# Kernel optimization log

Measured on AMD Instinct MI355X. Metric: run time of the kernel, lower is better.

The kernel has to match this reference:

```python
import jax, jax.numpy as jnp
import numpy as np

B, S, C, H = 2, 4096, 1024, 8
D = C // H
KCONV = 7  # depthwise causal conv kernel size


def setup_inputs() -> dict:
    key = jax.random.key(0)
    k1, k2, k3, k4 = jax.random.split(key, 4)
    x = jax.random.normal(k1, (B, S, C), jnp.float32)
    Wqkv = jax.random.normal(k2, (C, 3 * C), jnp.float32) * (1.0 / np.sqrt(C))
    Wo = jax.random.normal(k3, (C, C), jnp.float32) * (1.0 / np.sqrt(C))
    conv_w = jax.random.normal(k4, (C, KCONV), jnp.float32) * (1.0 / np.sqrt(KCONV))
    return {"x": x, "Wqkv": Wqkv, "Wo": Wo, "conv_w": conv_w}


def _ripple(x, Wqkv, Wo, conv_w):
    b, s, c = x.shape
    d = c // H
    qkv = x @ Wqkv
    q, k, v = jnp.split(qkv, 3, axis=-1)

    def heads(t):
        return t.reshape(b, s, H, d).transpose(0, 2, 1, 3)  # [B,H,S,D]

    qh, kh, vh = heads(q), heads(k), heads(v)

    # --- branch 1: telescoping attention (offsets 0, 1, 2, 4, ..., 2^k) ---
    n_pow = int(np.floor(np.log2(s))) + 1
    offsets = jnp.concatenate([jnp.zeros((1,), jnp.int32),
                               (2 ** jnp.arange(n_pow)).astype(jnp.int32)])  # [K]
    pos = jnp.arange(s, dtype=jnp.int32)[:, None] - offsets[None, :]  # [S,K]
    valid = pos >= 0
    posc = jnp.clip(pos, 0)
    kg = kh[:, :, posc]  # [B,H,S,K,D] gathered keys
    vg = vh[:, :, posc]  # [B,H,S,K,D] gathered values
    sc = jnp.einsum('bhsd,bhskd->bhsk', qh, kg) / np.sqrt(d)
    sc = jnp.where(valid[None, None], sc, -jnp.inf)  # offset 0 always valid
    w = jax.nn.softmax(sc, axis=-1)
    tele = jnp.einsum('bhsk,bhskd->bhsd', w, vg)

    # --- branch 2: depthwise causal conv over value stream ---
    vpad = jnp.pad(v, ((0, 0), (KCONV - 1, 0), (0, 0)))  # left pad -> causal
    conv = jax.lax.conv_general_dilated(
        vpad.transpose(0, 2, 1),        # NCH
        conv_w[:, None, :],             # OIH, groups=C -> I=1
        window_strides=(1,), padding='VALID',
        feature_group_count=c,
        dimension_numbers=('NCH', 'OIH', 'NCH')).transpose(0, 2, 1)  # [B,S,C]
    conv_h = conv.reshape(b, s, H, d).transpose(0, 2, 1, 3)

    # --- branch 3: low-rank (linear) attention, elu+1 feature map ---
    fq = jax.nn.elu(qh) + 1.0
    fk = jax.nn.elu(kh) + 1.0
    kv = jnp.einsum('bhsd,bhse->bhde', fk, vh)        # [B,H,D,D]
    z = jnp.einsum('bhsd,bhd->bhs', fq, fk.sum(2))    # normalizer
    low = jnp.einsum('bhsd,bhde->bhse', fq, kv) / (z[..., None] + 1e-6)

    h = (tele + conv_h + low).transpose(0, 2, 1, 3).reshape(b, s, c)
    return h @ Wo


def reference(x, Wqkv, Wo, conv_w):
    # RippleAttentionBlock: h, _ = ripple_attn(x); return x + h
    return x + _ripple(x, Wqkv, Wo, conv_w)
```

## Files before the change

kernel.cpp:

```cpp
#include <hip/hip_runtime.h>
#include <hip/hip_bf16.h>

#define BATCH 2
#define SEQ   4096
#define CHN   1024
#define NH    8
#define HD    128
#define NQROWS (BATCH*SEQ)
#define QKVN  (3*CHN)
#define NOFF  14
#define KCONV 7
#define NCH   16
#define CHS   (SEQ/NCH)
#define SLICE ((size_t)SEQ*HD)

typedef short bf16x8v __attribute__((ext_vector_type(8)));
typedef short bf16x4v __attribute__((ext_vector_type(4)));
typedef float f32x4v  __attribute__((ext_vector_type(4)));

__device__ __forceinline__ float b2f(short s) {
    return __uint_as_float(((unsigned)(unsigned short)s) << 16);
}
__device__ __forceinline__ unsigned short f2bu(float f) {
    __hip_bfloat16 h = __float2bfloat16(f);
    return *reinterpret_cast<unsigned short*>(&h);
}
__device__ __forceinline__ void gload16(const void* g, void* l) {
    __builtin_amdgcn_global_load_lds(
        (const __attribute__((address_space(1))) unsigned int*)g,
        (__attribute__((address_space(3))) unsigned int*)l, 16, 0, 0);
}

__global__ void k_cvt(const float* __restrict__ in, short* __restrict__ out, int n4) {
    int i = blockIdx.x * blockDim.x + threadIdx.x;
    int stride = gridDim.x * blockDim.x;
    for (; i < n4; i += stride) {
        float4 v = reinterpret_cast<const float4*>(in)[i];
        ushort4 o;
        o.x = f2bu(v.x); o.y = f2bu(v.y); o.z = f2bu(v.z); o.w = f2bu(v.w);
        reinterpret_cast<ushort4*>(out)[i] = o;
    }
}

__global__ void k_transpose_cvt(const float* __restrict__ in, short* __restrict__ out,
                                int R, int Cc) {
    __shared__ float tile[32][33];
    int bc = blockIdx.x * 32, br = blockIdx.y * 32;
    int tx = threadIdx.x & 31, ty = threadIdx.x >> 5;
    for (int i = 0; i < 32; i += 8)
        tile[ty + i][tx] = in[(size_t)(br + ty + i) * Cc + bc + tx];
    __syncthreads();
    for (int i = 0; i < 32; i += 8)
        out[(size_t)(bc + ty + i) * R + br + tx] = (short)f2bu(tile[tx][ty + i]);
}

template<int EPI>
__global__ __launch_bounds__(256)
void k_gemm_bt(const short* __restrict__ A, const short* __restrict__ Bt,
               short* __restrict__ Cb, float* __restrict__ Cf,
               const float* __restrict__ resid, int M, int N, int K) {
    __shared__ short As[128 * 32];
    __shared__ short Bs[128 * 32];
    int tid = threadIdx.x;
    int w = tid >> 6, lane = tid & 63;
    int nbn = N >> 7;
    int bm = blockIdx.x / nbn, bn = blockIdx.x % nbn;
    size_t m0 = (size_t)bm << 7, n0 = (size_t)bn << 7;
    int wr = (w >> 1) << 6, wc = (w & 1) << 6;
    int lr = lane & 15, lk = lane >> 4;
    f32x4v acc[4][4] = {};

    int f0 = w * 64 + lane, f1 = f0 + 256;
    int r0 = f0 >> 2, q0 = f0 & 3;
    int r1 = f1 >> 2, q1 = f1 & 3;
    const short* Ap0 = A + (m0 + r0) * K + q0 * 8;
    const short* Ap1 = A + (m0 + r1) * K + q1 * 8;
    const short* Bp0 = Bt + (n0 + r0) * K + q0 * 8;
    const short* Bp1 = Bt + (n0 + r1) * K + q1 * 8;
    short* Asl0 = As + (w * 64) * 8;
    short* Asl1 = As + (256 + w * 64) * 8;
    short* Bsl0 = Bs + (w * 64) * 8;
    short* Bsl1 = Bs + (256 + w * 64) * 8;

    for (int k0 = 0; k0 < K; k0 += 32) {
        gload16(Ap0 + k0, Asl0);
        gload16(Ap1 + k0, Asl1);
        gload16(Bp0 + k0, Bsl0);
        gload16(Bp1 + k0, Bsl1);
        __syncthreads();
        bf16x8v af[4], bfv[4];
        #pragma unroll
        for (int m = 0; m < 4; ++m)
            af[m] = *reinterpret_cast<const bf16x8v*>(As + (wr + m * 16 + lr) * 32 + lk * 8);
        #pragma unroll
        for (int n = 0; n < 4; ++n)
            bfv[n] = *reinterpret_cast<const bf16x8v*>(Bs + (wc + n * 16 + lr) * 32 + lk * 8);
        #pragma unroll
        for (int m = 0; m < 4; ++m)
            #pragma unroll
            for (int n = 0; n < 4; ++n)
                acc[m][n] = __builtin_amdgcn_mfma_f32_16x16x32_bf16(af[m], bfv[n], acc[m][n], 0, 0, 0);
        __syncthreads();
    }
    #pragma unroll
    for (int m = 0; m < 4; ++m) {
        size_t grow = m0 + wr + m * 16 + lk * 4;
        #pragma unroll
        for (int n = 0; n < 4; ++n) {
            size_t gcol = n0 + wc + n * 16 + lr;
            if (EPI == 0) {
                int bq = (int)(grow >> 12);
                int tq = (int)(gcol >> 10);
                int hh = ((int)gcol >> 7) & 7;
                int d  = (int)gcol & 127;
                size_t base = ((size_t)(tq * 2 + bq) * 8 + hh) * SLICE + d;
                #pragma unroll
                for (int i = 0; i < 4; ++i) {
                    size_t s = (grow + i) & 4095;
                    Cb[base + s * 128] = (short)f2bu(acc[m][n][i]);
                }
            } else {
                #pragma unroll
                for (int i = 0; i < 4; ++i) {
                    size_t idx = (grow + i) * N + gcol;
                    Cf[idx] = resid[idx] + acc[m][n][i];
                }
            }
        }
    }
}

__global__ __launch_bounds__(256)
void k_kvpart(const short* __restrict__ qkvs, float* __restrict__ kvpart,
              float* __restrict__ kspart) {
    __shared__ float fk_lds[32 * 128];
    __shared__ short v_lds[32 * 64];
    int t = threadIdx.x;
    int w = t >> 6, lane = t & 63;
    int bid = blockIdx.x;
    int eh = bid & 1;
    int ch = (bid >> 1) & (NCH - 1);
    int bh = bid / (NCH * 2);
    int b = bh >> 3, h = bh & 7;
    const short* kbase = qkvs + ((size_t)(2 + b) * 8 + h) * SLICE;
    const short* vbase = qkvs + ((size_t)(4 + b) * 8 + h) * SLICE + eh * 64;
    int s0 = ch * CHS;
    int d0 = (t >> 4) * 8;
    int e0l = (t & 15) * 4;
    float kv[8][4] = {};
    float ks[8] = {};
    for (int sub = 0; sub < CHS / 32; ++sub) {
        #pragma unroll
        for (int j = 0; j < 2; ++j) {
            int f = j * 256 + t;
            int row = f >> 4, c0 = (f & 15) * 8;
            bf16x8v k8 = *reinterpret_cast<const bf16x8v*>(
                kbase + (size_t)(s0 + sub * 32 + row) * HD + c0);
            float* dst = fk_lds + row * 128 + c0;
            #pragma unroll
            for (int e = 0; e < 8; ++e) {
                float x = b2f(k8[e]);
                dst[e] = x > 0.f ? x + 1.f : __expf(x);
            }
        }
        {
            int f = w * 64 + lane;
            gload16(vbase + (size_t)(s0 + sub * 32 + (f >> 3)) * HD + (f & 7) * 8,
                    v_lds + (size_t)(w * 64) * 8);
        }
        __syncthreads();
        for (int ss = 0; ss < 32; ++ss) {
            float fa[8];
            *(float4*)&fa[0] = *(const float4*)&fk_lds[ss * 128 + d0];
            *(float4*)&fa[4] = *(const float4*)&fk_lds[ss * 128 + d0 + 4];
            bf16x4v vv = *reinterpret_cast<const bf16x4v*>(&v_lds[ss * 64 + e0l]);
            float vb[4];
            #pragma unroll
            for (int e = 0; e < 4; ++e) vb[e] = b2f(vv[e]);
            #pragma unroll
            for (int i = 0; i < 8; ++i) {
                ks[i] += fa[i];
                #pragma unroll
                for (int e = 0; e < 4; ++e) kv[i][e] += fa[i] * vb[e];
            }
        }
        __syncthreads();
    }
    size_t obase = (size_t)bid * (128 * 64);
    #pragma unroll
    for (int i = 0; i < 8; ++i)
        *(float4*)&kvpart[obase + (d0 + i) * 64 + e0l] = *(float4*)&kv[i][0];
    if ((t & 15) == 0 && eh == 0)
        #pragma unroll
        for (int i = 0; i < 8; ++i)
            kspart[(size_t)(bh * NCH + ch) * 128 + d0 + i] = ks[i];
}

__global__ void k_kvreduce(const float* __restrict__ kvpart, const float* __restrict__ kspart,
                           short* __restrict__ kvt, float* __restrict__ ksum) {
    int idx = blockIdx.x * blockDim.x + threadIdx.x;
    const int total_kv = 16 * 128 * 128;
    if (idx < total_kv) {
        int bh = idx >> 14;
        int r = idx & 16383;
        int d = r >> 7, e = r & 127;
        int ehalf = e >> 6, el = e & 63;
        float s = 0.f;
        const float* p = kvpart + ((size_t)(bh * NCH) * 2 + ehalf) * 8192 + d * 64 + el;
        #pragma unroll
        for (int c = 0; c < NCH; ++c) s += p[(size_t)c * 2 * 8192];
        kvt[((size_t)bh << 14) + e * 128 + d] = (short)f2bu(s);
    } else {
        int k = idx - total_kv;
        if (k < 16 * 128) {
            int bh = k >> 7, d = k & 127;
            float s = 0.f;
            const float* p = kspart + (size_t)bh * NCH * 128 + d;
            #pragma unroll
            for (int c = 0; c < NCH; ++c) s += p[c * 128];
            ksum[k] = s;
        }
    }
}

__global__ __launch_bounds__(256)
void k_middle(const short* __restrict__ qkvs, const short* __restrict__ kvt,
              const float* __restrict__ ksum, const float* __restrict__ conv_w,
              short* __restrict__ hbuf) {
    __shared__ short fq_lds[32 * 128];
    __shared__ float low_lds[32 * 128];
    __shared__ float ksum_lds[128];
    __shared__ float cw_lds[128 * KCONV];
    int t = threadIdx.x;
    int w = t >> 6, lane = t & 63;
    int bid = blockIdx.x;
    int bh = bid >> 7, chunk = bid & 127;
    int b = bh >> 3, h = bh & 7;
    int s0 = chunk * 32;
    const short* qbase = qkvs + ((size_t)(0 + b) * 8 + h) * SLICE;
    const short* kbase = qkvs + ((size_t)(2 + b) * 8 + h) * SLICE;
    const short* vbase = qkvs + ((size_t)(4 + b) * 8 + h) * SLICE;

    if (t < 128) ksum_lds[t] = ksum[bh * 128 + t];
    for (int f = t; f < 128 * KCONV; f += 256) {
        int d = f / KCONV, j = f % KCONV;
        cw_lds[f] = conv_w[(h * HD + d) * KCONV + j];
    }
    #pragma unroll
    for (int j = 0; j < 2; ++j) {
        int f = j * 256 + t;
        int row = f >> 4, c0 = (f & 15) * 8;
        bf16x8v q8 = *reinterpret_cast<const bf16x8v*>(
            qbase + (size_t)(s0 + row) * HD + c0);
        bf16x8v fq8;
        #pragma unroll
        for (int e = 0; e < 8; ++e) {
            float x = b2f(q8[e]);
            float fx = x > 0.f ? x + 1.f : __expf(x);
            fq8[e] = (short)f2bu(fx);
        }
        *reinterpret_cast<bf16x8v*>(fq_lds + row * 128 + c0) = fq8;
    }
    __syncthreads();
    {
        int lr = lane & 15, lk = lane >> 4;
        const short* kvg = kvt + ((size_t)bh << 14);
        f32x4v lacc[2][2] = {};
        #pragma unroll
        for (int ksb = 0; ksb < 4; ++ksb) {
            bf16x8v af[2], bfv[2];
            #pragma unroll
            for (int m = 0; m < 2; ++m)
                af[m] = *reinterpret_cast<const bf16x8v*>(fq_lds + (m * 16 + lr) * 128 + ksb * 32 + lk * 8);
            #pragma unroll
            for (int n = 0; n < 2; ++n)
                bfv[n] = *reinterpret_cast<const bf16x8v*>(kvg + (w * 32 + n * 16 + lr) * 128 + ksb * 32 + lk * 8);
            #pragma unroll
            for (int m = 0; m < 2; ++m)
                #pragma unroll
                for (int n = 0; n < 2; ++n)
                    lacc[m][n] = __builtin_amdgcn_mfma_f32_16x16x32_bf16(af[m], bfv[n], lacc[m][n], 0, 0, 0);
        }
        #pragma unroll
        for (int m = 0; m < 2; ++m)
            #pragma unroll
            for (int n = 0; n < 2; ++n)
                #pragma unroll
                for (int i = 0; i < 4; ++i)
                    low_lds[(m * 16 + lk * 4 + i) * 128 + w * 32 + n * 16 + lr] = lacc[m][n][i];
    }
    int row = t >> 3, j8 = t & 7;
    int e0 = j8 * 16;
    int sl = s0 + row;
    float zp = 0.f;
    #pragma unroll
    for (int d = 0; d < 16; ++d)
        zp += b2f(fq_lds[row * 128 + e0 + d]) * ksum_lds[e0 + d];
    zp += __shfl_xor(zp, 1); zp += __shfl_xor(zp, 2); zp += __shfl_xor(zp, 4);
    float z = zp + 1e-6f;
    float qv[16];
    {
        const short* qp = qbase + (size_t)sl * HD + e0;
        bf16x8v q0 = *(const bf16x8v*)qp;
        bf16x8v q1 = *(const bf16x8v*)(qp + 8);
        #pragma unroll
        for (int d = 0; d < 8; ++d) { qv[d] = b2f(q0[d]); qv[8 + d] = b2f(q1[d]); }
    }
    float scb[NOFF];
    #pragma unroll
    for (int o = 0; o < NOFF; ++o) {
        int off = (o == 0) ? 0 : (1 << (o - 1));
        int p = sl - off;
        float acc = 0.f;
        if (p >= 0) {
            const short* kp = kbase + (size_t)p * HD + e0;
            bf16x8v k0v = *(const bf16x8v*)kp;
            bf16x8v k1v = *(const bf16x8v*)(kp + 8);
            #pragma unroll
            for (int d = 0; d < 8; ++d) acc += qv[d] * b2f(k0v[d]);
            #pragma unroll
            for (int d = 0; d < 8; ++d) acc += qv[8 + d] * b2f(k1v[d]);
        }
        scb[o] = acc;
    }
    #pragma unroll
    for (int o = 0; o < NOFF; ++o) {
        float v = scb[o];
        v += __shfl_xor(v, 1); v += __shfl_xor(v, 2); v += __shfl_xor(v, 4);
        scb[o] = v * 0.08838834764831845f;
    }
    float mmax = -1e30f;
    #pragma unroll
    for (int o = 0; o < NOFF; ++o) {
        int off = (o == 0) ? 0 : (1 << (o - 1));
        if (sl - off >= 0 && scb[o] > mmax) mmax = scb[o];
    }
    float wsum = 0.f;
    float tacc[16] = {};
    #pragma unroll
    for (int o = 0; o < NOFF; ++o) {
        int off = (o == 0) ? 0 : (1 << (o - 1));
        int p = sl - off;
        if (p < 0) continue;
        float wv = __expf(scb[o] - mmax);
        wsum += wv;
        const short* vp = vbase + (size_t)p * HD + e0;
        bf16x8v v0 = *(const bf16x8v*)vp;
        bf16x8v v1 = *(const bf16x8v*)(vp + 8);
        #pragma unroll
        for (int d = 0; d < 8; ++d) tacc[d]     += wv * b2f(v0[d]);
        #pragma unroll
        for (int d = 0; d < 8; ++d) tacc[8 + d] += wv * b2f(v1[d]);
    }
    float inv_wsum = 1.f / wsum;
    float cacc[16] = {};
    #pragma unroll
    for (int jj = 0; jj < KCONV; ++jj) {
        int p = sl - 6 + jj;
        if (p < 0) continue;
        const short* vp = vbase + (size_t)p * HD + e0;
        bf16x8v v0 = *(const bf16x8v*)vp;
        bf16x8v v1 = *(const bf16x8v*)(vp + 8);
        #pragma unroll
        for (int d = 0; d < 8; ++d) cacc[d]     += b2f(v0[d]) * cw_lds[(e0 + d) * KCONV + jj];
        #pragma unroll
        for (int d = 0; d < 8; ++d) cacc[8 + d] += b2f(v1[d]) * cw_lds[(e0 + 8 + d) * KCONV + jj];
    }
    __syncthreads();
    short outv[16];
    #pragma unroll
    for (int d = 0; d < 16; ++d) {
        float hval = tacc[d] * inv_wsum + cacc[d] + low_lds[row * 128 + e0 + d] / z;
        outv[d] = (short)f2bu(hval);
    }
    bf16x8v* op = (bf16x8v*)(hbuf + ((size_t)b * SEQ + sl) * CHN + h * HD + e0);
    op[0] = *(bf16x8v*)&outv[0];
    op[1] = *(bf16x8v*)&outv[8];
}

extern "C" void kernel_launch(void* const* d_in, const int* in_sizes, int n_in,
                              void* d_out, int out_size, void* d_ws, size_t ws_size,
                              hipStream_t stream) {
    const float* x      = (const float*)d_in[0];
    const float* Wqkv   = (const float*)d_in[1];
    const float* Wo     = (const float*)d_in[2];
    const float* conv_w = (const float*)d_in[3];
    float* out = (float*)d_out;

    char* ws = (char*)d_ws;
    size_t off = 0;
    auto alloc = [&](size_t bytes) {
        char* p = ws + off;
        off += (bytes + 255) & ~(size_t)255;
        return (void*)p;
    };
    short* xb     = (short*)alloc((size_t)NQROWS * CHN * 2);
    short* wqkvT  = (short*)alloc((size_t)QKVN * CHN * 2);
    short* woT    = (short*)alloc((size_t)CHN * CHN * 2);
    short* qkvs   = (short*)alloc((size_t)3 * BATCH * NH * SEQ * HD * 2);
    short* hbuf   = (short*)alloc((size_t)NQROWS * CHN * 2);
    float* kvpart = (float*)alloc((size_t)16 * NCH * 2 * 128 * 64 * 4);
    float* kspart = (float*)alloc((size_t)16 * NCH * 128 * 4);
    short* kvt    = (short*)alloc((size_t)16 * 128 * 128 * 2);
    float* ksum   = (float*)alloc((size_t)16 * 128 * 4);

    k_cvt<<<2048, 256, 0, stream>>>(x, xb, NQROWS * CHN / 4);
    k_transpose_cvt<<<dim3(QKVN / 32, CHN / 32), 256, 0, stream>>>(Wqkv, wqkvT, CHN, QKVN);
    k_transpose_cvt<<<dim3(CHN / 32, CHN / 32), 256, 0, stream>>>(Wo, woT, CHN, CHN);
    k_gemm_bt<0><<<(NQROWS / 128) * (QKVN / 128), 256, 0, stream>>>(
        xb, wqkvT, qkvs, nullptr, nullptr, NQROWS, QKVN, CHN);
    k_kvpart<<<16 * NCH * 2, 256, 0, stream>>>(qkvs, kvpart, kspart);
    k_kvreduce<<<(16 * 128 * 128 + 16 * 128) / 256, 256, 0, stream>>>(kvpart, kspart, kvt, ksum);
    k_middle<<<16 * 128, 256, 0, stream>>>(qkvs, kvt, ksum, conv_w, hbuf);
    k_gemm_bt<1><<<(NQROWS / 128) * (CHN / 128), 256, 0, stream>>>(
        hbuf, woT, nullptr, out, x, NQROWS, CHN, CHN);
}
```

Measured before the change: 298.9 us.

## Compute linear-attention KV partials with MFMA and split ksum into separate kernel

Replaces the scalar FMA outer-product KV accumulation with a bf16 MFMA kernel. It stages transposed, XOR-swizzled feature-mapped keys and values in LDS, uses 32 sequence chunks, and writes full 128x128 partials. The key-sum normalizer moves to its own small kernel. Both GEMMs are split into two launches over half the rows each via an m_off parameter. Feeding the feature-mapped keys to the MFMA as bf16 loses some precision, the KV partial buffer grows, and the split GEMMs add launch overhead.

```diff
diff --git a/kernel.cpp b/kernel.cpp
--- a/kernel.cpp
+++ b/kernel.cpp
@@ -10,12 +10,11 @@
 #define QKVN  (3*CHN)
 #define NOFF  14
 #define KCONV 7
-#define NCH   16
-#define CHS   (SEQ/NCH)
+#define NCH2  32
+#define CHS2  (SEQ/NCH2)
 #define SLICE ((size_t)SEQ*HD)
 
 typedef short bf16x8v __attribute__((ext_vector_type(8)));
-typedef short bf16x4v __attribute__((ext_vector_type(4)));
 typedef float f32x4v  __attribute__((ext_vector_type(4)));
 
 __device__ __forceinline__ float b2f(short s) {
@@ -58,14 +57,14 @@
 __global__ __launch_bounds__(256)
 void k_gemm_bt(const short* __restrict__ A, const short* __restrict__ Bt,
                short* __restrict__ Cb, float* __restrict__ Cf,
-               const float* __restrict__ resid, int M, int N, int K) {
+               const float* __restrict__ resid, int N, int K, int m_off) {
     __shared__ short As[128 * 32];
     __shared__ short Bs[128 * 32];
     int tid = threadIdx.x;
     int w = tid >> 6, lane = tid & 63;
     int nbn = N >> 7;
     int bm = blockIdx.x / nbn, bn = blockIdx.x % nbn;
-    size_t m0 = (size_t)bm << 7, n0 = (size_t)bn << 7;
+    size_t m0 = ((size_t)bm << 7) + m_off, n0 = (size_t)bn << 7;
     int wr = (w >> 1) << 6, wc = (w & 1) << 6;
     int lr = lane & 15, lk = lane >> 4;
     f32x4v acc[4][4] = {};
@@ -131,69 +130,84 @@
 }
 
 __global__ __launch_bounds__(256)
-void k_kvpart(const short* __restrict__ qkvs, float* __restrict__ kvpart,
-              float* __restrict__ kspart) {
-    __shared__ float fk_lds[32 * 128];
-    __shared__ short v_lds[32 * 64];
+void k_kvpart_mfma(const short* __restrict__ qkvs, float* __restrict__ kvpart) {
+    __shared__ short fkt[128 * 32];
+    __shared__ short vt[128 * 32];
     int t = threadIdx.x;
     int w = t >> 6, lane = t & 63;
+    int lr = lane & 15, lk = lane >> 4;
+    int bh = blockIdx.x >> 5, ch = blockIdx.x & 31;
+    int b = bh >> 3, h = bh & 7;
+    const short* kb = qkvs + ((size_t)(2 + b) * 8 + h) * SLICE;
+    const short* vb = qkvs + ((size_t)(4 + b) * 8 + h) * SLICE;
+    int s0 = ch * CHS2;
+    int dq = (w >> 1) * 64, eq = (w & 1) * 64;
+    int g16 = (t & 7) * 16;
+    int sl  = t >> 3;
+    f32x4v acc[4][4] = {};
+
+    for (int sub = 0; sub < CHS2 / 32; ++sub) {
+        int srow = s0 + sub * 32 + sl;
+        const short* kp = kb + (size_t)srow * HD + g16;
+        const short* vp = vb + (size_t)srow * HD + g16;
+        bf16x8v k0 = *(const bf16x8v*)kp, k1 = *(const bf16x8v*)(kp + 8);
+        bf16x8v v0 = *(const bf16x8v*)vp, v1 = *(const bf16x8v*)(vp + 8);
+        #pragma unroll
+        for (int jj = 0; jj < 16; ++jj) {
+            int d = g16 + jj;
+            float kx = b2f(jj < 8 ? k0[jj] : k1[jj - 8]);
+            float fkv = kx > 0.f ? kx + 1.f : __expf(kx);
+            int byte = (d * 64 + sl * 2) ^ ((jj & 7) << 4);
+            *(short*)((char*)fkt + byte) = (short)f2bu(fkv);
+            *(short*)((char*)vt  + byte) = (jj < 8 ? v0[jj] : v1[jj - 8]);
+        }
+        __syncthreads();
+        bf16x8v af[4], bfv[4];
+        #pragma unroll
+        for (int m = 0; m < 4; ++m) {
+            int byte = ((dq + m * 16 + lr) * 64 + lk * 16) ^ ((lr & 7) << 4);
+            af[m] = *(const bf16x8v*)((const char*)fkt + byte);
+        }
+        #pragma unroll
+        for (int n = 0; n < 4; ++n) {
+            int byte = ((eq + n * 16 + lr) * 64 + lk * 16) ^ ((lr & 7) << 4);
+            bfv[n] = *(const bf16x8v*)((const char*)vt + byte);
+        }
+        #pragma unroll
+        for (int m = 0; m < 4; ++m)
+            #pragma unroll
+            for (int n = 0; n < 4; ++n)
+                acc[m][n] = __builtin_amdgcn_mfma_f32_16x16x32_bf16(af[m], bfv[n], acc[m][n], 0, 0, 0);
+        __syncthreads();
+    }
+    size_t obase = (size_t)blockIdx.x * 16384;
+    #pragma unroll
+    for (int m = 0; m < 4; ++m) {
+        int dr = dq + m * 16 + lk * 4;
+        #pragma unroll
+        for (int n = 0; n < 4; ++n) {
+            int ec = eq + n * 16 + lr;
+            #pragma unroll
+            for (int i = 0; i < 4; ++i)
+                kvpart[obase + (size_t)(dr + i) * 128 + ec] = acc[m][n][i];
+        }
+    }
+}
+
+__global__ __launch_bounds__(128)
+void k_ksum(const short* __restrict__ qkvs, float* __restrict__ kspart) {
     int bid = blockIdx.x;
-    int eh = bid & 1;
-    int ch = (bid >> 1) & (NCH - 1);
-    int bh = bid / (NCH * 2);
+    int bh = bid >> 4, cs = bid & 15;
     int b = bh >> 3, h = bh & 7;
-    const short* kbase = qkvs + ((size_t)(2 + b) * 8 + h) * SLICE;
-    const short* vbase = qkvs + ((size_t)(4 + b) * 8 + h) * SLICE + eh * 64;
-    int s0 = ch * CHS;
-    int d0 = (t >> 4) * 8;
-    int e0l = (t & 15) * 4;
-    float kv[8][4] = {};
-    float ks[8] = {};
-    for (int sub = 0; sub < CHS / 32; ++sub) {
-        #pragma unroll
-        for (int j = 0; j < 2; ++j) {
-            int f = j * 256 + t;
-            int row = f >> 4, c0 = (f & 15) * 8;
-            bf16x8v k8 = *reinterpret_cast<const bf16x8v*>(
-                kbase + (size_t)(s0 + sub * 32 + row) * HD + c0);
-            float* dst = fk_lds + row * 128 + c0;
-            #pragma unroll
-            for (int e = 0; e < 8; ++e) {
-                float x = b2f(k8[e]);
-                dst[e] = x > 0.f ? x + 1.f : __expf(x);
-            }
-        }
-        {
-            int f = w * 64 + lane;
-            gload16(vbase + (size_t)(s0 + sub * 32 + (f >> 3)) * HD + (f & 7) * 8,
-                    v_lds + (size_t)(w * 64) * 8);
-        }
-        __syncthreads();
-        for (int ss = 0; ss < 32; ++ss) {
-            float fa[8];
-            *(float4*)&fa[0] = *(const float4*)&fk_lds[ss * 128 + d0];
-            *(float4*)&fa[4] = *(const float4*)&fk_lds[ss * 128 + d0 + 4];
-            bf16x4v vv = *reinterpret_cast<const bf16x4v*>(&v_lds[ss * 64 + e0l]);
-            float vb[4];
-            #pragma unroll
-            for (int e = 0; e < 4; ++e) vb[e] = b2f(vv[e]);
-            #pragma unroll
-            for (int i = 0; i < 8; ++i) {
-                ks[i] += fa[i];
-                #pragma unroll
-                for (int e = 0; e < 4; ++e) kv[i][e] += fa[i] * vb[e];
-            }
-        }
-        __syncthreads();
-    }
-    size_t obase = (size_t)bid * (128 * 64);
-    #pragma unroll
-    for (int i = 0; i < 8; ++i)
-        *(float4*)&kvpart[obase + (d0 + i) * 64 + e0l] = *(float4*)&kv[i][0];
-    if ((t & 15) == 0 && eh == 0)
-        #pragma unroll
-        for (int i = 0; i < 8; ++i)
-            kspart[(size_t)(bh * NCH + ch) * 128 + d0 + i] = ks[i];
+    int d = threadIdx.x;
+    const short* kb = qkvs + ((size_t)(2 + b) * 8 + h) * SLICE + (size_t)(cs * 256) * HD;
+    float s = 0.f;
+    #pragma unroll 4
+    for (int i = 0; i < 256; ++i) {
+        float x = b2f(kb[(size_t)i * HD + d]);
+        s += x > 0.f ? x + 1.f : __expf(x);
+    }
+    kspart[bid * 128 + d] = s;
 }
 
 __global__ void k_kvreduce(const float* __restrict__ kvpart, const float* __restrict__ kspart,
@@ -204,20 +218,19 @@
         int bh = idx >> 14;
         int r = idx & 16383;
         int d = r >> 7, e = r & 127;
-        int ehalf = e >> 6, el = e & 63;
         float s = 0.f;
-        const float* p = kvpart + ((size_t)(bh * NCH) * 2 + ehalf) * 8192 + d * 64 + el;
-        #pragma unroll
-        for (int c = 0; c < NCH; ++c) s += p[(size_t)c * 2 * 8192];
+        const float* p = kvpart + ((size_t)bh * NCH2) * 16384 + r;
+        #pragma unroll
+        for (int c = 0; c < NCH2; ++c) s += p[(size_t)c * 16384];
         kvt[((size_t)bh << 14) + e * 128 + d] = (short)f2bu(s);
     } else {
         int k = idx - total_kv;
         if (k < 16 * 128) {
             int bh = k >> 7, d = k & 127;
             float s = 0.f;
-            const float* p = kspart + (size_t)bh * NCH * 128 + d;
-            #pragma unroll
-            for (int c = 0; c < NCH; ++c) s += p[c * 128];
+            const float* p = kspart + (size_t)bh * 16 * 128 + d;
+            #pragma unroll
+            for (int c = 0; c < 16; ++c) s += p[c * 128];
             ksum[k] = s;
         }
     }
@@ -399,19 +412,24 @@
     short* woT    = (short*)alloc((size_t)CHN * CHN * 2);
     short* qkvs   = (short*)alloc((size_t)3 * BATCH * NH * SEQ * HD * 2);
     short* hbuf   = (short*)alloc((size_t)NQROWS * CHN * 2);
-    float* kvpart = (float*)alloc((size_t)16 * NCH * 2 * 128 * 64 * 4);
-    float* kspart = (float*)alloc((size_t)16 * NCH * 128 * 4);
+    float* kvpart = (float*)alloc((size_t)16 * NCH2 * 128 * 128 * 4);
+    float* kspart = (float*)alloc((size_t)16 * 16 * 128 * 4);
     short* kvt    = (short*)alloc((size_t)16 * 128 * 128 * 2);
     float* ksum   = (float*)alloc((size_t)16 * 128 * 4);
 
     k_cvt<<<2048, 256, 0, stream>>>(x, xb, NQROWS * CHN / 4);
     k_transpose_cvt<<<dim3(QKVN / 32, CHN / 32), 256, 0, stream>>>(Wqkv, wqkvT, CHN, QKVN);
     k_transpose_cvt<<<dim3(CHN / 32, CHN / 32), 256, 0, stream>>>(Wo, woT, CHN, CHN);
-    k_gemm_bt<0><<<(NQROWS / 128) * (QKVN / 128), 256, 0, stream>>>(
-        xb, wqkvT, qkvs, nullptr, nullptr, NQROWS, QKVN, CHN);
-    k_kvpart<<<16 * NCH * 2, 256, 0, stream>>>(qkvs, kvpart, kspart);
+    k_gemm_bt<0><<<(4096 / 128) * (QKVN / 128), 256, 0, stream>>>(
+        xb, wqkvT, qkvs, nullptr, nullptr, QKVN, CHN, 0);
+    k_gemm_bt<0><<<(4096 / 128) * (QKVN / 128), 256, 0, stream>>>(
+        xb, wqkvT, qkvs, nullptr, nullptr, QKVN, CHN, 4096);
+    k_kvpart_mfma<<<16 * NCH2, 256, 0, stream>>>(qkvs, kvpart);
+    k_ksum<<<16 * 16, 128, 0, stream>>>(qkvs, kspart);
     k_kvreduce<<<(16 * 128 * 128 + 16 * 128) / 256, 256, 0, stream>>>(kvpart, kspart, kvt, ksum);
     k_middle<<<16 * 128, 256, 0, stream>>>(qkvs, kvt, ksum, conv_w, hbuf);
-    k_gemm_bt<1><<<(NQROWS / 128) * (CHN / 128), 256, 0, stream>>>(
-        hbuf, woT, nullptr, out, x, NQROWS, CHN, CHN);
-}
+    k_gemm_bt<1><<<(4096 / 128) * (CHN / 128), 256, 0, stream>>>(
+        hbuf, woT, nullptr, out, x, CHN, CHN, 0);
+    k_gemm_bt<1><<<(4096 / 128) * (CHN / 128), 256, 0, stream>>>(
+        hbuf, woT, nullptr, out, x, CHN, CHN, 4096);
+}
```

Result: slower. 327.5 us (+9.5%).
